# Performance work log

Hardware: AMD Instinct MI355X
Metric: run time of the kernel (lower is better)

The kernel has to match this reference:

```python
import jax, jax.numpy as jnp
import numpy as np

B, T, D = 32, 256, 64

def setup_inputs() -> dict:
    key = jax.random.key(0)
    k1, k2 = jax.random.split(key)
    real = jax.random.normal(k1, (B, T, D), dtype=jnp.float32)
    imag = jax.random.normal(k2, (B, T, D), dtype=jnp.float32)
    return {"real": real, "imag": imag}

def reference(real, imag):
    # Original: transpose(0,1) then, per (t, b), form complex v = r + i*j and the
    # outer product v v^H of shape [D, D]; stack over b; list over t.
    # Vectorized: out[t, b, p, q] = v[t,b,p] * conj(v[t,b,q])
    #   real part = r_p r_q + i_p i_q
    #   imag part = i_p r_q - r_p i_q
    r = jnp.transpose(real, (1, 0, 2))  # [T, B, D]
    im = jnp.transpose(imag, (1, 0, 2))  # [T, B, D]
    out_real = jnp.einsum('tbp,tbq->tbpq', r, r) + jnp.einsum('tbp,tbq->tbpq', im, im)
    out_imag = jnp.einsum('tbp,tbq->tbpq', im, r) - jnp.einsum('tbp,tbq->tbpq', r, im)
    # Stack real/imag parts instead of complex dtype: [2, T, B, D, D]
    return jnp.stack([out_real, out_imag], axis=0)
```

## Files before the change

kernel.cpp:

```cpp
#include <hip/hip_runtime.h>


namespace {
constexpr int kB = 32;
constexpr int kT = 256;
constexpr int kD = 64;
constexpr int kDD = kD * kD;
}

__global__ __launch_bounds__(256) void qouter_kernel(
    const float* __restrict__ real,
    const float* __restrict__ imag,
    float* __restrict__ out) {
    const int blk = blockIdx.x;
    const int t = blk / kB;
    const int b = blk % kB;

    __shared__ float sr[kD];
    __shared__ float si[kD];

    const int tid = threadIdx.x;
    const int in_base = (b * kT + t) * kD;
    if (tid < kD) {
        sr[tid] = real[in_base + tid];
    } else if (tid < 2 * kD) {
        si[tid - kD] = imag[in_base + (tid - kD)];
    }
    __syncthreads();

    const size_t base_r = ((size_t)t * kB + b) * kDD;
    const size_t base_i = base_r + (size_t)kT * kB * kDD;
    float4* __restrict__ outr = (float4*)(out + base_r);
    float4* __restrict__ outi = (float4*)(out + base_i);
    const float4* __restrict__ sr4 = (const float4*)sr;
    const float4* __restrict__ si4 = (const float4*)si;

#pragma unroll
    for (int k = 0; k < 4; ++k) {
        const int idx = tid + k * 256;
        const int p = idx >> 4;
        const int j = idx & 15;
        const float rp = sr[p];
        const float ip = si[p];
        const float4 rq = sr4[j];
        const float4 iq = si4[j];
        float4 vr, vi;
        vr.x = rp * rq.x + ip * iq.x;
        vr.y = rp * rq.y + ip * iq.y;
        vr.z = rp * rq.z + ip * iq.z;
        vr.w = rp * rq.w + ip * iq.w;
        vi.x = ip * rq.x - rp * iq.x;
        vi.y = ip * rq.y - rp * iq.y;
        vi.z = ip * rq.z - rp * iq.z;
        vi.w = ip * rq.w - rp * iq.w;
        outr[idx] = vr;
        outi[idx] = vi;
    }
}

extern "C" void kernel_launch(void* const* d_in, const int* in_sizes, int n_in,
                              void* d_out, int out_size, void* d_ws, size_t ws_size,
                              hipStream_t stream) {
    const float* real = (const float*)d_in[0];
    const float* imag = (const float*)d_in[1];
    float* out = (float*)d_out;
    qouter_kernel<<<kT * kB, 256, 0, stream>>>(real, imag, out);
}
```

Before: 261.6 us.

## Use one wave per (t,b) pair with shuffles, nontemporal stores, persistent grid

Each 64-lane wave now handles a whole (t,b) outer product, broadcasting the row values with wave shuffles instead of staging them in shared memory and synchronising the block. Output is written with nontemporal vector stores to avoid polluting the cache with the 268MB write stream. The grid is reduced to 2048 blocks that loop over pairs with a grid stride. This mainly targets store efficiency in a write-bandwidth-bound kernel, at the cost of shuffle overhead and fewer resident waves.

```diff
diff --git a/kernel.cpp b/kernel.cpp
--- a/kernel.cpp
+++ b/kernel.cpp
@@ -1,60 +1,58 @@
 #include <hip/hip_runtime.h>
 
+
+typedef float v4f __attribute__((ext_vector_type(4)));
 
 namespace {
 constexpr int kB = 32;
 constexpr int kT = 256;
 constexpr int kD = 64;
 constexpr int kDD = kD * kD;
+constexpr int kPairs = kT * kB;
 }
 
 __global__ __launch_bounds__(256) void qouter_kernel(
     const float* __restrict__ real,
     const float* __restrict__ imag,
     float* __restrict__ out) {
-    const int blk = blockIdx.x;
-    const int t = blk / kB;
-    const int b = blk % kB;
+    const int lane = threadIdx.x & 63;
+    const int wavesPerBlock = blockDim.x >> 6;
+    const int wid = blockIdx.x * wavesPerBlock + (threadIdx.x >> 6);
+    const int nwaves = gridDim.x * wavesPerBlock;
 
-    __shared__ float sr[kD];
-    __shared__ float si[kD];
+    for (int pair = wid; pair < kPairs; pair += nwaves) {
+        const int t = pair >> 5;
+        const int b = pair & (kB - 1);
+        const int in_base = (b * kT + t) * kD;
 
-    const int tid = threadIdx.x;
-    const int in_base = (b * kT + t) * kD;
-    if (tid < kD) {
-        sr[tid] = real[in_base + tid];
-    } else if (tid < 2 * kD) {
-        si[tid - kD] = imag[in_base + (tid - kD)];
-    }
-    __syncthreads();
+        const float rv = real[in_base + lane];
+        const float iv = imag[in_base + lane];
+        const int j = lane & 15;
+        const v4f rq = *(const v4f*)(real + in_base + 4 * j);
+        const v4f iq = *(const v4f*)(imag + in_base + 4 * j);
 
-    const size_t base_r = ((size_t)t * kB + b) * kDD;
-    const size_t base_i = base_r + (size_t)kT * kB * kDD;
-    float4* __restrict__ outr = (float4*)(out + base_r);
-    float4* __restrict__ outi = (float4*)(out + base_i);
-    const float4* __restrict__ sr4 = (const float4*)sr;
-    const float4* __restrict__ si4 = (const float4*)si;
+        v4f* __restrict__ outr = (v4f*)(out + (size_t)pair * kDD);
+        v4f* __restrict__ outi = (v4f*)(out + (size_t)pair * kDD
+                                        + (size_t)kPairs * kDD);
 
 #pragma unroll
-    for (int k = 0; k < 4; ++k) {
-        const int idx = tid + k * 256;
-        const int p = idx >> 4;
-        const int j = idx & 15;
-        const float rp = sr[p];
-        const float ip = si[p];
-        const float4 rq = sr4[j];
-        const float4 iq = si4[j];
-        float4 vr, vi;
-        vr.x = rp * rq.x + ip * iq.x;
-        vr.y = rp * rq.y + ip * iq.y;
-        vr.z = rp * rq.z + ip * iq.z;
-        vr.w = rp * rq.w + ip * iq.w;
-        vi.x = ip * rq.x - rp * iq.x;
-        vi.y = ip * rq.y - rp * iq.y;
-        vi.z = ip * rq.z - rp * iq.z;
-        vi.w = ip * rq.w - rp * iq.w;
-        outr[idx] = vr;
-        outi[idx] = vi;
+        for (int it = 0; it < 16; ++it) {
+            const int idx = it * 64 + lane;
+            const int p = idx >> 4;
+            const float rp = __shfl(rv, p);
+            const float ip = __shfl(iv, p);
+            v4f vr, vi;
+            vr.x = rp * rq.x + ip * iq.x;
+            vr.y = rp * rq.y + ip * iq.y;
+            vr.z = rp * rq.z + ip * iq.z;
+            vr.w = rp * rq.w + ip * iq.w;
+            vi.x = ip * rq.x - rp * iq.x;
+            vi.y = ip * rq.y - rp * iq.y;
+            vi.z = ip * rq.z - rp * iq.z;
+            vi.w = ip * rq.w - rp * iq.w;
+            __builtin_nontemporal_store(vr, outr + idx);
+            __builtin_nontemporal_store(vi, outi + idx);
+        }
     }
 }
 
@@ -64,5 +62,5 @@
     const float* real = (const float*)d_in[0];
     const float* imag = (const float*)d_in[1];
     float* out = (float*)d_out;
-    qouter_kernel<<<kT * kB, 256, 0, stream>>>(real, imag, out);
+    qouter_kernel<<<2048, 256, 0, stream>>>(real, imag, out);
 }
```

Result: slower. 271.2 us (+3.7%).
